# Performance work log

Hardware: AMD Instinct MI355X
Metric: run time of the kernel (lower is better)

## Reference

```python
import jax, jax.numpy as jnp
import numpy as np

D = 768      # feature_dim
HD = 768     # hidden_dim
NH = 4       # num_heads
B, T1, T2 = 4, 128, 128
LN_EPS = 1e-5

def setup_inputs() -> dict:
    key = jax.random.key(0)
    ks = jax.random.split(key, 12)
    s = 0.02
    return {
        'speech_features': jax.random.normal(ks[0], (B, T1, D), jnp.float32),
        'phoneme_features': jax.random.normal(ks[1], (B, T2, D), jnp.float32),
        # per-head attention MLP: Linear(2D->HD), ReLU, Linear(HD->1); stacked over heads
        'W1': jax.random.normal(ks[2], (NH, 2 * D, HD), jnp.float32) * s,
        'b1': jnp.zeros((NH, HD), jnp.float32),
        'w2': jax.random.normal(ks[3], (NH, HD), jnp.float32) * s,
        'b2': jnp.zeros((NH,), jnp.float32),
        # fusion: Linear(2D->2HD), ReLU, Linear(2HD->D), LayerNorm(D)
        'Wf1': jax.random.normal(ks[4], (2 * D, 2 * HD), jnp.float32) * s,
        'bf1': jnp.zeros((2 * HD,), jnp.float32),
        'Wf2': jax.random.normal(ks[5], (2 * HD, D), jnp.float32) * s,
        'bf2': jnp.zeros((D,), jnp.float32),
        'ln_g': jnp.ones((D,), jnp.float32),
        'ln_b': jnp.zeros((D,), jnp.float32),
    }

def reference(speech_features, phoneme_features, W1, b1, w2, b2, Wf1, bf1, Wf2, bf2, ln_g, ln_b):
    d = speech_features.shape[-1]
    # Decompose Linear(cat([speech_t, phoneme])) = speech@W1[:d] + phoneme@W1[d:] + b1
    Wx, Wy = W1[:, :d, :], W1[:, d:, :]
    sx = jnp.einsum('btd,ndh->nbth', speech_features, Wx)   # [NH,B,T1,HD]
    py = jnp.einsum('bsd,ndh->nbsh', phoneme_features, Wy)  # [NH,B,T2,HD]
    hidden = jax.nn.relu(sx[:, :, :, None, :] + py[:, :, None, :, :]
                         + b1[:, None, None, None, :])      # [NH,B,T1,T2,HD]
    scores = jnp.einsum('nbtsh,nh->nbts', hidden, w2) + b2[:, None, None, None]
    attn = jax.nn.softmax(scores, axis=-1).mean(axis=0)     # [B,T1,T2]
    context = jnp.einsum('bts,bsd->btd', attn, phoneme_features)  # [B,T1,D]
    fused = jnp.concatenate([speech_features, context], axis=-1)  # [B,T1,2D]
    # dropout is identity in eval mode
    h = jax.nn.relu(fused @ Wf1 + bf1)
    out = h @ Wf2 + bf2
    mu = out.mean(axis=-1, keepdims=True)
    var = ((out - mu) ** 2).mean(axis=-1, keepdims=True)
    out = (out - mu) * jax.lax.rsqrt(var + LN_EPS) * ln_g + ln_b
    return out.mean(axis=1)  # [B,D]
```

## Files before the change

kernel.cpp:

```cpp
#include <hip/hip_runtime.h>
#include <cstddef>


#define D_  768
#define HD_ 768
#define NH_ 4
#define B_  4
#define T1_ 128
#define T2_ 128
#define M_  (B_*T1_)
#define LN_EPS_ 1e-5f

typedef unsigned short u16;
typedef unsigned int u32;
typedef _Float16 f16;
typedef _Float16 f16x2 __attribute__((ext_vector_type(2)));
typedef __bf16 bf16x8 __attribute__((ext_vector_type(8)));
typedef float f32x4 __attribute__((ext_vector_type(4)));

__device__ __forceinline__ u16 f2bf(float f) {
    union { float f; unsigned int u; } v; v.f = f;
    unsigned int u = v.u + (0x7FFFu + ((v.u >> 16) & 1u));
    return (u16)(u >> 16);
}
__device__ __forceinline__ u32 pack_bf2(float lo, float hi) {
    return (u32)f2bf(lo) | ((u32)f2bf(hi) << 16);
}
__device__ __forceinline__ u16 f16bits(f16 h) {
    return __builtin_bit_cast(unsigned short, h);
}
__device__ __forceinline__ f16x2 bcast2(u32 u) {
    return __builtin_bit_cast(f16x2, u);
}
__device__ __forceinline__ u32 splat2(u16 h) { return (u32)h * 0x10001u; }

template<bool RELU, int MODE, bool AF32, bool SPLIT>
__device__ __forceinline__ void gemm_mfma_body(
    const void* __restrict__ Av1, const void* __restrict__ Av2, int lda,
    const u16* __restrict__ Bt, int ldb,
    const float* __restrict__ bias,
    void* __restrict__ C, int ldc, int K, int m0, int n0)
{
    __shared__ __align__(16) u16 As[64][40];
    __shared__ __align__(16) u16 Bs[64][40];
    __shared__ u16 Ts[MODE == 3 ? 64 : 1][MODE == 3 ? 68 : 1];

    const int tid = threadIdx.x;
    const int row = tid >> 2;
    const int kq  = (tid & 3) << 3;
    const int lane = tid & 63;
    const int w  = tid >> 6;
    const int wr = (w >> 1) << 5;
    const int wc = (w & 1) << 5;
    const int l16 = lane & 15;
    const int lk8 = (lane >> 4) << 3;
    const int r4  = (lane >> 4) << 2;

    const u16*   aptr16  = (const u16*)Av1 + (size_t)(m0 + row) * lda + kq;
    const float* aptrf1  = (const float*)Av1 + (size_t)(m0 + row) * lda + kq;
    const float* aptrf2  = SPLIT ? ((const float*)Av2 + (size_t)(m0 + row) * lda + kq) : nullptr;
    const u16*   bptr    = Bt + (size_t)(n0 + row) * ldb + kq;

    f32x4 acc00 = {0.f,0.f,0.f,0.f}, acc01 = {0.f,0.f,0.f,0.f};
    f32x4 acc10 = {0.f,0.f,0.f,0.f}, acc11 = {0.f,0.f,0.f,0.f};

    auto loadA = [&](int k0) -> uint4 {
        if (AF32) {
            const float* base = aptrf1;
            int kk = k0;
            if (SPLIT && k0 >= 768) { base = aptrf2; kk = k0 - 768; }
            float4 ax = *(const float4*)(base + kk);
            float4 ay = *(const float4*)(base + kk + 4);
            uint4 r;
            r.x = pack_bf2(ax.x, ax.y); r.y = pack_bf2(ax.z, ax.w);
            r.z = pack_bf2(ay.x, ay.y); r.w = pack_bf2(ay.z, ay.w);
            return r;
        }
        return *(const uint4*)(aptr16 + k0);
    };

    uint4 a_nxt = loadA(0);
    uint4 b_nxt = *(const uint4*)bptr;

    for (int k0 = 0; k0 < K; k0 += 32) {
        __syncthreads();
        *(uint4*)&As[row][kq] = a_nxt;
        *(uint4*)&Bs[row][kq] = b_nxt;
        if (k0 + 32 < K) {
            a_nxt = loadA(k0 + 32);
            b_nxt = *(const uint4*)(bptr + k0 + 32);
        }
        __syncthreads();
        bf16x8 af0 = *(const bf16x8*)&As[wr + l16][lk8];
        bf16x8 af1 = *(const bf16x8*)&As[wr + 16 + l16][lk8];
        bf16x8 bf0 = *(const bf16x8*)&Bs[wc + l16][lk8];
        bf16x8 bf1 = *(const bf16x8*)&Bs[wc + 16 + l16][lk8];
        acc00 = __builtin_amdgcn_mfma_f32_16x16x32_bf16(af0, bf0, acc00, 0, 0, 0);
        acc01 = __builtin_amdgcn_mfma_f32_16x16x32_bf16(af0, bf1, acc01, 0, 0, 0);
        acc10 = __builtin_amdgcn_mfma_f32_16x16x32_bf16(af1, bf0, acc10, 0, 0, 0);
        acc11 = __builtin_amdgcn_mfma_f32_16x16x32_bf16(af1, bf1, acc11, 0, 0, 0);
    }

#define EPI_FRAG(ACC, MF, NF)                                                  \
    {                                                                          \
        const int gcol = n0 + wc + (NF)*16 + l16;                              \
        const float bv = bias ? bias[gcol] : 0.f;                              \
        float v_[4];                                                           \
        _Pragma("unroll")                                                      \
        for (int r = 0; r < 4; r++) {                                          \
            float v = ACC[r] + bv;                                             \
            if (RELU) v = fmaxf(v, 0.f);                                       \
            v_[r] = v;                                                         \
        }                                                                      \
        const int lr0 = wr + (MF)*16 + r4;                                     \
        if (MODE == 3) {                                                       \
            const int lc = wc + (NF)*16 + l16;                                 \
            _Pragma("unroll")                                                  \
            for (int r = 0; r < 4; r++) Ts[lc][lr0 + r] = f16bits((f16)v_[r]); \
        } else {                                                               \
            _Pragma("unroll")                                                  \
            for (int r = 0; r < 4; r++) {                                      \
                const size_t off = (size_t)(m0 + lr0 + r) * ldc + gcol;        \
                if (MODE == 0) ((float*)C)[off] = v_[r];                       \
                else if (MODE == 1) ((u16*)C)[off] = f2bf(v_[r]);              \
                else ((u16*)C)[off] = f16bits((f16)v_[r]);                     \
            }                                                                  \
        }                                                                      \
    }
    EPI_FRAG(acc00, 0, 0) EPI_FRAG(acc01, 0, 1)
    EPI_FRAG(acc10, 1, 0) EPI_FRAG(acc11, 1, 1)
#undef EPI_FRAG

    if (MODE == 3) {
        __syncthreads();
        u16* cb = (u16*)C + (size_t)(m0 >> 7) * (768 * 128) + (m0 & 127);
#pragma unroll
        for (int u = 0; u < 4; u++) {
            const int i = tid + u * 256;
            const int hl = i >> 4;
            const int s4 = (i & 15) << 2;
            ushort4 o;
            o.x = Ts[hl][s4 + 0]; o.y = Ts[hl][s4 + 1];
            o.z = Ts[hl][s4 + 2]; o.w = Ts[hl][s4 + 3];
            *(ushort4*)(cb + (size_t)(n0 + hl) * 128 + s4) = o;
        }
    }
}

__global__ __launch_bounds__(256) void prep_kernel(
    const float* __restrict__ W1, const float* __restrict__ Wf1,
    const float* __restrict__ Wf2,
    u16* __restrict__ w1t, u16* __restrict__ wf1t, u16* __restrict__ wf2t)
{
    const int tid = threadIdx.x;
    int bid = blockIdx.x;
    const float* in; u16* outp; int tx, ty;
    if (bid < 4608) {
        const int z = bid / 1152, r = bid % 1152;
        tx = r % 24; ty = r / 24;
        in = W1 + (size_t)z * 1536 * 768; outp = w1t + (size_t)z * 768 * 1536;
    } else if (bid < 6912) {
        const int r = bid - 4608;
        tx = r % 48; ty = r / 48;
        in = Wf1; outp = wf1t;
    } else {
        const int r = bid - 6912;
        tx = r % 24; ty = r / 24;
        in = Wf2; outp = wf2t;
    }
    const int C = (bid >= 4608 && bid < 6912) ? 1536 : 768;
    const int c0 = tx * 32, r0 = ty * 32;
    __shared__ float tile[32][33];
    const int tr = tid >> 3, tc = (tid & 7) << 2;
    float4 v = *(const float4*)(in + (size_t)(r0 + tr) * C + c0 + tc);
    tile[tr][tc] = v.x; tile[tr][tc + 1] = v.y;
    tile[tr][tc + 2] = v.z; tile[tr][tc + 3] = v.w;
    __syncthreads();
    ushort4 o;
    o.x = f2bf(tile[tc + 0][tr]); o.y = f2bf(tile[tc + 1][tr]);
    o.z = f2bf(tile[tc + 2][tr]); o.w = f2bf(tile[tc + 3][tr]);
    *(ushort4*)(outp + (size_t)(c0 + tr) * 1536 + r0 + tc) = o;
}

__global__ __launch_bounds__(256) void gemm_sxpy_kernel(
    const float* __restrict__ sp, const float* __restrict__ ph,
    const u16* __restrict__ w1t, const float* __restrict__ b1,
    u16* __restrict__ sxf, u16* __restrict__ pyt)
{
    const int z = blockIdx.z;
    const int n = z & 3;
    const bool ispy = z >= 4;
    const u16* Bt = w1t + (size_t)n * 768 * 1536 + (ispy ? 768 : 0);
    if (!ispy) {
        gemm_mfma_body<false, 2, true, false>(sp, nullptr, 768, Bt, 1536, b1 + n * HD_,
                                              sxf + (size_t)n * M_ * HD_, HD_, 768,
                                              blockIdx.y * 64, blockIdx.x * 64);
    } else {
        gemm_mfma_body<false, 3, true, false>(ph, nullptr, 768, Bt, 1536, nullptr,
                                              pyt + (size_t)n * 4 * 768 * 128, 0, 768,
                                              blockIdx.y * 64, blockIdx.x * 64);
    }
}

__global__ __launch_bounds__(256) void gemm_ffn1_kernel(
    const float* __restrict__ speech, const float* __restrict__ ctx,
    const u16* __restrict__ wf1t, const float* __restrict__ bf1,
    u16* __restrict__ hbuf)
{
    gemm_mfma_body<true, 1, true, true>(speech, ctx, 768, wf1t, 1536, bf1,
                                        hbuf, 1536, 1536,
                                        blockIdx.y * 64, blockIdx.x * 64);
}

__global__ __launch_bounds__(256) void gemm_ffn2_kernel(
    const u16* __restrict__ hbuf, const u16* __restrict__ wf2t,
    const float* __restrict__ bf2, float* __restrict__ outpre)
{
    gemm_mfma_body<false, 0, false, false>(hbuf, nullptr, 1536, wf2t, 1536, bf2,
                                           outpre, 768, 1536,
                                           blockIdx.y * 64, blockIdx.x * 64);
}

__global__ __launch_bounds__(256) void scores_softmax_kernel(
    const u16* __restrict__ sxf,
    const u16* __restrict__ pyt,
    const float* __restrict__ w2,
    float* __restrict__ probs)
{
    const int bid = blockIdx.x;
    const int n = bid >> 6, b = (bid >> 4) & 3, t0 = (bid & 15) * 8;
    const int tid = threadIdx.x, lane = tid & 63, w = tid >> 6;

    __shared__ __align__(16) f16x2 sxs[8][768];
    __shared__ __align__(16) f16x2 w2s[768];

    for (int q = 0; q < 6; q++) {
        const int u = tid + q * 256;
        const int r = u / 192;
        const int h4 = (u % 192) * 4;
        ushort4 v = *(const ushort4*)(sxf + ((size_t)(n * 512 + b * 128 + t0 + r)) * 768 + h4);
        sxs[r][h4 + 0] = bcast2(splat2(v.x));
        sxs[r][h4 + 1] = bcast2(splat2(v.y));
        sxs[r][h4 + 2] = bcast2(splat2(v.z));
        sxs[r][h4 + 3] = bcast2(splat2(v.w));
    }
    for (int q = 0; q < 3; q++) {
        const int i = tid + q * 256;
        w2s[i] = bcast2(splat2(f16bits((f16)w2[n * 768 + i])));
    }
    __syncthreads();

    const f16x2* pypanel = (const f16x2*)(pyt + ((size_t)((n << 2) | b)) * 768 * 128) + lane;
    const f16x2 z2 = {(f16)0, (f16)0};

    float accA0 = 0.f, accA1 = 0.f, accB0 = 0.f, accB1 = 0.f;
    const int rA = 2 * w, rB = 2 * w + 1;

    f16x2 b0[16], b1[16];
#pragma unroll
    for (int j = 0; j < 16; j++) b0[j] = pypanel[(size_t)j * 64];
#pragma unroll
    for (int j = 0; j < 16; j++) b1[j] = pypanel[(size_t)(16 + j) * 64];

    auto compute = [&](const f16x2 (&buf)[16], int hbase) {
        f16x2 aA = z2, aB = z2;
#pragma unroll
        for (int j4 = 0; j4 < 16; j4 += 4) {
            uint4 sau = *(const uint4*)&sxs[rA][hbase + j4];
            uint4 sbu = *(const uint4*)&sxs[rB][hbase + j4];
            uint4 wvu = *(const uint4*)&w2s[hbase + j4];
            const u32 sa_[4] = {sau.x, sau.y, sau.z, sau.w};
            const u32 sb_[4] = {sbu.x, sbu.y, sbu.z, sbu.w};
            const u32 wv_[4] = {wvu.x, wvu.y, wvu.z, wvu.w};
#pragma unroll
            for (int j = 0; j < 4; j++) {
                const f16x2 pv = buf[j4 + j];
                const f16x2 wj = bcast2(wv_[j]);
                f16x2 ra = __builtin_elementwise_max(bcast2(sa_[j]) + pv, z2);
                f16x2 rb = __builtin_elementwise_max(bcast2(sb_[j]) + pv, z2);
                aA = __builtin_elementwise_fma(ra, wj, aA);
                aB = __builtin_elementwise_fma(rb, wj, aB);
            }
        }
        accA0 += (float)aA.x; accA1 += (float)aA.y;
        accB0 += (float)aB.x; accB1 += (float)aB.y;
    };

    for (int hc = 0; hc < 768; hc += 32) {
        compute(b0, hc);
        if (hc + 32 < 768) {
#pragma unroll
            for (int j = 0; j < 16; j++) b0[j] = pypanel[(size_t)(hc + 32 + j) * 64];
        }
        compute(b1, hc + 16);
        if (hc + 48 < 768) {
#pragma unroll
            for (int j = 0; j < 16; j++) b1[j] = pypanel[(size_t)(hc + 48 + j) * 64];
        }
    }

#pragma unroll
    for (int which = 0; which < 2; which++) {
        const float s0 = which ? accB0 : accA0;
        const float s1 = which ? accB1 : accA1;
        const int t = t0 + 2 * w + which;
        float mx = fmaxf(s0, s1);
#pragma unroll
        for (int off = 32; off; off >>= 1) mx = fmaxf(mx, __shfl_xor(mx, off, 64));
        const float e0 = expf(s0 - mx), e1 = expf(s1 - mx);
        float sm = e0 + e1;
#pragma unroll
        for (int off = 32; off; off >>= 1) sm += __shfl_xor(sm, off, 64);
        const float inv = 0.25f / sm;
        float2 pr; pr.x = e0 * inv; pr.y = e1 * inv;
        *(float2*)&probs[((size_t)(n * 512 + b * 128 + t)) * 128 + 2 * lane] = pr;
    }
}

__global__ __launch_bounds__(256) void context_kernel(
    const float* __restrict__ probs, const float* __restrict__ phon,
    float* __restrict__ ctx)
{
    const int m = blockIdx.x;
    const int b = m >> 7;
    const int tid = threadIdx.x;
    __shared__ float attn[T2_];
    if (tid < T2_) {
        float a = 0.f;
#pragma unroll
        for (int n = 0; n < NH_; n++)
            a += probs[(size_t)(n * M_ + m) * T2_ + tid];
        attn[tid] = a;
    }
    __syncthreads();
    const float* ph = phon + (size_t)b * T2_ * D_;
#pragma unroll
    for (int j = 0; j < 3; j++) {
        const int d = tid + 256 * j;
        float acc = 0.f;
#pragma unroll 8
        for (int s = 0; s < T2_; s++)
            acc = fmaf(attn[s], ph[(size_t)s * D_ + d], acc);
        ctx[(size_t)m * D_ + d] = acc;
    }
}

__global__ __launch_bounds__(256) void ln_fused_kernel(
    const float* __restrict__ x, const float* __restrict__ g,
    const float* __restrict__ lb, float* __restrict__ out)
{
    const int b = blockIdx.x / 3, c = blockIdx.x % 3;
    const int tid = threadIdx.x, lane = tid & 63, w = tid >> 6;
    __shared__ float rs[T1_];
    __shared__ float Sred[4];

    float prsum = 0.f;
    for (int i = 0; i < 32; i++) {
        const int row = w * 32 + i;
        const float4* x4 = (const float4*)(x + ((size_t)(b * T1_ + row)) * D_);
        float s = 0.f, ss = 0.f;
#pragma unroll
        for (int j = 0; j < 3; j++) {
            float4 v = x4[j * 64 + lane];
            s += v.x + v.y + v.z + v.w;
            ss += v.x * v.x + v.y * v.y + v.z * v.z + v.w * v.w;
        }
#pragma unroll
        for (int off = 32; off; off >>= 1) {
            s += __shfl_xor(s, off, 64);
            ss += __shfl_xor(ss, off, 64);
        }
        if (lane == 0) {
            const float mu = s * (1.f / D_);
            const float var = ss * (1.f / D_) - mu * mu;
            const float r = rsqrtf(var + LN_EPS_);
            rs[row] = r;
            prsum += mu * r;
        }
    }
    if (lane == 0) Sred[w] = prsum;
    __syncthreads();
    const float S = Sred[0] + Sred[1] + Sred[2] + Sred[3];
    const float* xb = x + (size_t)b * T1_ * D_;
    const int d = c * 256 + tid;
    float acc = 0.f;
#pragma unroll 8
    for (int t = 0; t < T1_; t++)
        acc = fmaf(xb[(size_t)t * D_ + d], rs[t], acc);
    out[b * D_ + d] = g[d] * (acc - S) * (1.f / T1_) + lb[d];
}

extern "C" void kernel_launch(void* const* d_in, const int* in_sizes, int n_in,
                              void* d_out, int out_size, void* d_ws, size_t ws_size,
                              hipStream_t stream)
{
    const float* speech = (const float*)d_in[0];
    const float* phon   = (const float*)d_in[1];
    const float* W1     = (const float*)d_in[2];
    const float* b1     = (const float*)d_in[3];
    const float* w2     = (const float*)d_in[4];
    const float* Wf1    = (const float*)d_in[6];
    const float* bf1    = (const float*)d_in[7];
    const float* Wf2    = (const float*)d_in[8];
    const float* bf2    = (const float*)d_in[9];
    const float* ln_g   = (const float*)d_in[10];
    const float* ln_b   = (const float*)d_in[11];
    float* out = (float*)d_out;

    char* w = (char*)d_ws;
    auto alloc = [&](size_t bytes) { char* p = w; w += (bytes + 1023) & ~(size_t)1023; return p; };
    u16* w1t    = (u16*)alloc((size_t)NH_ * 768 * 1536 * 2);
    u16* wf1t   = (u16*)alloc((size_t)1536 * 1536 * 2);
    u16* wf2t   = (u16*)alloc((size_t)768 * 1536 * 2);
    u16* sxf    = (u16*)alloc((size_t)NH_ * M_ * HD_ * 2);
    u16* pyt    = (u16*)alloc((size_t)NH_ * B_ * 768 * 128 * 2);
    float* probs  = (float*)alloc((size_t)NH_ * M_ * T2_ * 4);
    float* ctxb   = (float*)alloc((size_t)M_ * D_ * 4);
    u16* hbuf   = (u16*)alloc((size_t)M_ * 2 * HD_ * 2);
    float* outpre = (float*)alloc((size_t)M_ * D_ * 4);

    hipLaunchKernelGGL(prep_kernel, dim3(8064), dim3(256), 0, stream,
                       W1, Wf1, Wf2, w1t, wf1t, wf2t);
    hipLaunchKernelGGL(gemm_sxpy_kernel, dim3(HD_ / 64, M_ / 64, 8), dim3(256), 0, stream,
                       speech, phon, w1t, b1, sxf, pyt);
    hipLaunchKernelGGL(scores_softmax_kernel, dim3(256), dim3(256), 0, stream,
                       sxf, pyt, w2, probs);
    hipLaunchKernelGGL(context_kernel, dim3(M_), dim3(256), 0, stream,
                       probs, phon, ctxb);
    hipLaunchKernelGGL(gemm_ffn1_kernel, dim3(2 * HD_ / 64, M_ / 64), dim3(256), 0, stream,
                       speech, ctxb, wf1t, bf1, hbuf);
    hipLaunchKernelGGL(gemm_ffn2_kernel, dim3(D_ / 64, M_ / 64), dim3(256), 0, stream,
                       hbuf, wf2t, bf2, outpre);
    hipLaunchKernelGGL(ln_fused_kernel, dim3(12), dim3(256), 0, stream,
                       outpre, ln_g, ln_b, out);
}
```

Before: 142.6 us.

## Reassociate context@Wf1 as attn@(phoneme@Wf1y) and drop context kernel

Instead of computing context = attn @ phoneme and then feeding it through the second half of Wf1 (K=768), the code precomputes per-batch P = phoneme @ Wf1[768:] in the first GEMM launch and makes FFN1 consume the head-summed attention probabilities directly (K=128). This removes the context kernel, its fp32 buffer, and shrinks the FFN1 reduction from 1536 to 896, at the cost of an extra 4x128x1536 GEMM and rounding the attention weights and P to bf16. The sx, py and new P GEMMs are merged into one flat-grid launch.

Result: faster. 129.5 us (-9.2%).

```diff
diff --git a/kernel.cpp b/kernel.cpp
--- a/kernel.cpp
+++ b/kernel.cpp
@@ -34,16 +34,16 @@
 }
 __device__ __forceinline__ u32 splat2(u16 h) { return (u32)h * 0x10001u; }
 
-template<bool RELU, int MODE, bool AF32, bool SPLIT>
+template<bool RELU, int MODE, bool AF32>
 __device__ __forceinline__ void gemm_mfma_body(
-    const void* __restrict__ Av1, const void* __restrict__ Av2, int lda,
+    const void* __restrict__ Av, int lda,
     const u16* __restrict__ Bt, int ldb,
     const float* __restrict__ bias,
     void* __restrict__ C, int ldc, int K, int m0, int n0)
 {
     __shared__ __align__(16) u16 As[64][40];
     __shared__ __align__(16) u16 Bs[64][40];
-    __shared__ u16 Ts[MODE == 3 ? 64 : 1][MODE == 3 ? 68 : 1];
+    __shared__ u16 Ts[MODE >= 3 ? 64 : 1][MODE >= 3 ? 68 : 1];
 
     const int tid = threadIdx.x;
     const int row = tid >> 2;
@@ -56,21 +56,17 @@
     const int lk8 = (lane >> 4) << 3;
     const int r4  = (lane >> 4) << 2;
 
-    const u16*   aptr16  = (const u16*)Av1 + (size_t)(m0 + row) * lda + kq;
-    const float* aptrf1  = (const float*)Av1 + (size_t)(m0 + row) * lda + kq;
-    const float* aptrf2  = SPLIT ? ((const float*)Av2 + (size_t)(m0 + row) * lda + kq) : nullptr;
-    const u16*   bptr    = Bt + (size_t)(n0 + row) * ldb + kq;
+    const u16*   aptr16 = (const u16*)Av + (size_t)(m0 + row) * lda + kq;
+    const float* aptrf  = (const float*)Av + (size_t)(m0 + row) * lda + kq;
+    const u16*   bptr   = Bt + (size_t)(n0 + row) * ldb + kq;
 
     f32x4 acc00 = {0.f,0.f,0.f,0.f}, acc01 = {0.f,0.f,0.f,0.f};
     f32x4 acc10 = {0.f,0.f,0.f,0.f}, acc11 = {0.f,0.f,0.f,0.f};
 
     auto loadA = [&](int k0) -> uint4 {
         if (AF32) {
-            const float* base = aptrf1;
-            int kk = k0;
-            if (SPLIT && k0 >= 768) { base = aptrf2; kk = k0 - 768; }
-            float4 ax = *(const float4*)(base + kk);
-            float4 ay = *(const float4*)(base + kk + 4);
+            float4 ax = *(const float4*)(aptrf + k0);
+            float4 ay = *(const float4*)(aptrf + k0 + 4);
             uint4 r;
             r.x = pack_bf2(ax.x, ax.y); r.y = pack_bf2(ax.z, ax.w);
             r.z = pack_bf2(ay.x, ay.y); r.w = pack_bf2(ay.z, ay.w);
@@ -113,10 +109,12 @@
             v_[r] = v;                                                         \
         }                                                                      \
         const int lr0 = wr + (MF)*16 + r4;                                     \
-        if (MODE == 3) {                                                       \
+        if (MODE >= 3) {                                                       \
             const int lc = wc + (NF)*16 + l16;                                 \
             _Pragma("unroll")                                                  \
-            for (int r = 0; r < 4; r++) Ts[lc][lr0 + r] = f16bits((f16)v_[r]); \
+            for (int r = 0; r < 4; r++)                                        \
+                Ts[lc][lr0 + r] = (MODE == 3) ? f16bits((f16)v_[r])            \
+                                              : f2bf(v_[r]);                   \
         } else {                                                               \
             _Pragma("unroll")                                                  \
             for (int r = 0; r < 4; r++) {                                      \
@@ -131,9 +129,9 @@
     EPI_FRAG(acc10, 1, 0) EPI_FRAG(acc11, 1, 1)
 #undef EPI_FRAG
 
-    if (MODE == 3) {
+    if (MODE >= 3) {
         __syncthreads();
-        u16* cb = (u16*)C + (size_t)(m0 >> 7) * (768 * 128) + (m0 & 127);
+        u16* cb = (u16*)C + (size_t)(m0 >> 7) * ((size_t)ldc * 128) + (m0 & 127);
 #pragma unroll
         for (int u = 0; u < 4; u++) {
             const int i = tid + u * 256;
@@ -182,43 +180,31 @@
     *(ushort4*)(outp + (size_t)(c0 + tr) * 1536 + r0 + tc) = o;
 }
 
-__global__ __launch_bounds__(256) void gemm_sxpy_kernel(
+__global__ __launch_bounds__(256) void sxpypw_kernel(
     const float* __restrict__ sp, const float* __restrict__ ph,
-    const u16* __restrict__ w1t, const float* __restrict__ b1,
-    u16* __restrict__ sxf, u16* __restrict__ pyt)
-{
-    const int z = blockIdx.z;
-    const int n = z & 3;
-    const bool ispy = z >= 4;
-    const u16* Bt = w1t + (size_t)n * 768 * 1536 + (ispy ? 768 : 0);
-    if (!ispy) {
-        gemm_mfma_body<false, 2, true, false>(sp, nullptr, 768, Bt, 1536, b1 + n * HD_,
-                                              sxf + (size_t)n * M_ * HD_, HD_, 768,
-                                              blockIdx.y * 64, blockIdx.x * 64);
+    const u16* __restrict__ w1t, const u16* __restrict__ wf1t,
+    const float* __restrict__ b1,
+    u16* __restrict__ sxf, u16* __restrict__ pyt, u16* __restrict__ pwt)
+{
+    int job = blockIdx.x;
+    if (job < 384) {
+        const int n = job / 96, r = job % 96, my = r / 12, nx = r % 12;
+        gemm_mfma_body<false, 2, true>(sp, 768,
+            w1t + (size_t)n * 768 * 1536, 1536, b1 + n * HD_,
+            sxf + (size_t)n * M_ * HD_, HD_, 768, my * 64, nx * 64);
+    } else if (job < 768) {
+        const int j = job - 384;
+        const int n = j / 96, r = j % 96, my = r / 12, nx = r % 12;
+        gemm_mfma_body<false, 3, true>(ph, 768,
+            w1t + (size_t)n * 768 * 1536 + 768, 1536, nullptr,
+            pyt + (size_t)n * 4 * 768 * 128, 768, 768, my * 64, nx * 64);
     } else {
-        gemm_mfma_body<false, 3, true, false>(ph, nullptr, 768, Bt, 1536, nullptr,
-                                              pyt + (size_t)n * 4 * 768 * 128, 0, 768,
-                                              blockIdx.y * 64, blockIdx.x * 64);
-    }
-}
-
-__global__ __launch_bounds__(256) void gemm_ffn1_kernel(
-    const float* __restrict__ speech, const float* __restrict__ ctx,
-    const u16* __restrict__ wf1t, const float* __restrict__ bf1,
-    u16* __restrict__ hbuf)
-{
-    gemm_mfma_body<true, 1, true, true>(speech, ctx, 768, wf1t, 1536, bf1,
-                                        hbuf, 1536, 1536,
-                                        blockIdx.y * 64, blockIdx.x * 64);
-}
-
-__global__ __launch_bounds__(256) void gemm_ffn2_kernel(
-    const u16* __restrict__ hbuf, const u16* __restrict__ wf2t,
-    const float* __restrict__ bf2, float* __restrict__ outpre)
-{
-    gemm_mfma_body<false, 0, false, false>(hbuf, nullptr, 1536, wf2t, 1536, bf2,
-                                           outpre, 768, 1536,
-                                           blockIdx.y * 64, blockIdx.x * 64);
+        const int j = job - 768;
+        const int b = j / 48, r = j % 48, my = r / 24, nx = r % 24;
+        gemm_mfma_body<false, 4, true>(ph + (size_t)b * 128 * 768, 768,
+            wf1t + 768, 1536, nullptr,
+            pwt + (size_t)b * 1536 * 128, 1536, 768, my * 64, nx * 64);
+    }
 }
 
 __global__ __launch_bounds__(256) void scores_softmax_kernel(
@@ -317,32 +303,108 @@
     }
 }
 
-__global__ __launch_bounds__(256) void context_kernel(
-    const float* __restrict__ probs, const float* __restrict__ phon,
-    float* __restrict__ ctx)
-{
-    const int m = blockIdx.x;
-    const int b = m >> 7;
+__global__ __launch_bounds__(256) void gemm_ffn1_kernel(
+    const float* __restrict__ speech, const float* __restrict__ probs,
+    const u16* __restrict__ wf1t, const u16* __restrict__ pwt,
+    const float* __restrict__ bf1, u16* __restrict__ hbuf)
+{
+    __shared__ __align__(16) u16 As[64][40];
+    __shared__ __align__(16) u16 Bs[64][40];
+
     const int tid = threadIdx.x;
-    __shared__ float attn[T2_];
-    if (tid < T2_) {
-        float a = 0.f;
-#pragma unroll
-        for (int n = 0; n < NH_; n++)
-            a += probs[(size_t)(n * M_ + m) * T2_ + tid];
-        attn[tid] = a;
-    }
-    __syncthreads();
-    const float* ph = phon + (size_t)b * T2_ * D_;
-#pragma unroll
-    for (int j = 0; j < 3; j++) {
-        const int d = tid + 256 * j;
-        float acc = 0.f;
-#pragma unroll 8
-        for (int s = 0; s < T2_; s++)
-            acc = fmaf(attn[s], ph[(size_t)s * D_ + d], acc);
-        ctx[(size_t)m * D_ + d] = acc;
-    }
+    const int row = tid >> 2;
+    const int kq  = (tid & 3) << 3;
+    const int lane = tid & 63;
+    const int w  = tid >> 6;
+    const int wr = (w >> 1) << 5;
+    const int wc = (w & 1) << 5;
+    const int l16 = lane & 15;
+    const int lk8 = (lane >> 4) << 3;
+    const int r4  = (lane >> 4) << 2;
+
+    const int m0 = blockIdx.y * 64, n0 = blockIdx.x * 64;
+    const int b = m0 >> 7;
+
+    const float* arow = speech + (size_t)(m0 + row) * 768 + kq;
+    const float* prow = probs + (size_t)(m0 + row) * 128 + kq;
+    const u16* brow_w = wf1t + (size_t)(n0 + row) * 1536 + kq;
+    const u16* brow_p = pwt + (size_t)b * 1536 * 128 + (size_t)(n0 + row) * 128 + kq;
+
+    f32x4 acc00 = {0.f,0.f,0.f,0.f}, acc01 = {0.f,0.f,0.f,0.f};
+    f32x4 acc10 = {0.f,0.f,0.f,0.f}, acc11 = {0.f,0.f,0.f,0.f};
+
+    auto loadA = [&](int k0) -> uint4 {
+        uint4 r;
+        if (k0 < 768) {
+            float4 ax = *(const float4*)(arow + k0);
+            float4 ay = *(const float4*)(arow + k0 + 4);
+            r.x = pack_bf2(ax.x, ax.y); r.y = pack_bf2(ax.z, ax.w);
+            r.z = pack_bf2(ay.x, ay.y); r.w = pack_bf2(ay.z, ay.w);
+        } else {
+            const int ko = k0 - 768;
+            float4 ax = make_float4(0.f, 0.f, 0.f, 0.f), ay = ax;
+#pragma unroll
+            for (int n = 0; n < 4; n++) {
+                float4 u0 = *(const float4*)(prow + (size_t)n * 512 * 128 + ko);
+                float4 u1 = *(const float4*)(prow + (size_t)n * 512 * 128 + ko + 4);
+                ax.x += u0.x; ax.y += u0.y; ax.z += u0.z; ax.w += u0.w;
+                ay.x += u1.x; ay.y += u1.y; ay.z += u1.z; ay.w += u1.w;
+            }
+            r.x = pack_bf2(ax.x, ax.y); r.y = pack_bf2(ax.z, ax.w);
+            r.z = pack_bf2(ay.x, ay.y); r.w = pack_bf2(ay.z, ay.w);
+        }
+        return r;
+    };
+    auto loadB = [&](int k0) -> uint4 {
+        if (k0 < 768) return *(const uint4*)(brow_w + k0);
+        return *(const uint4*)(brow_p + (k0 - 768));
+    };
+
+    uint4 a_nxt = loadA(0);
+    uint4 b_nxt = loadB(0);
+
+    for (int k0 = 0; k0 < 896; k0 += 32) {
+        __syncthreads();
+        *(uint4*)&As[row][kq] = a_nxt;
+        *(uint4*)&Bs[row][kq] = b_nxt;
+        if (k0 + 32 < 896) {
+            a_nxt = loadA(k0 + 32);
+            b_nxt = loadB(k0 + 32);
+        }
+        __syncthreads();
+        bf16x8 af0 = *(const bf16x8*)&As[wr + l16][lk8];
+        bf16x8 af1 = *(const bf16x8*)&As[wr + 16 + l16][lk8];
+        bf16x8 bf0 = *(const bf16x8*)&Bs[wc + l16][lk8];
+        bf16x8 bf1 = *(const bf16x8*)&Bs[wc + 16 + l16][lk8];
+        acc00 = __builtin_amdgcn_mfma_f32_16x16x32_bf16(af0, bf0, acc00, 0, 0, 0);
+        acc01 = __builtin_amdgcn_mfma_f32_16x16x32_bf16(af0, bf1, acc01, 0, 0, 0);
+        acc10 = __builtin_amdgcn_mfma_f32_16x16x32_bf16(af1, bf0, acc10, 0, 0, 0);
+        acc11 = __builtin_amdgcn_mfma_f32_16x16x32_bf16(af1, bf1, acc11, 0, 0, 0);
+    }
+
+#define EPI_FFN1(ACC, MF, NF)                                                  \
+    {                                                                          \
+        const int gcol = n0 + wc + (NF)*16 + l16;                              \
+        const float bv = bf1[gcol];                                            \
+        const int lr0 = wr + (MF)*16 + r4;                                     \
+        _Pragma("unroll")                                                      \
+        for (int r = 0; r < 4; r++) {                                          \
+            float v = fmaxf(ACC[r] + bv, 0.f);                                 \
+            hbuf[(size_t)(m0 + lr0 + r) * 1536 + gcol] = f2bf(v);              \
+        }                                                                      \
+    }
+    EPI_FFN1(acc00, 0, 0) EPI_FFN1(acc01, 0, 1)
+    EPI_FFN1(acc10, 1, 0) EPI_FFN1(acc11, 1, 1)
+#undef EPI_FFN1
+}
+
+__global__ __launch_bounds__(256) void gemm_ffn2_kernel(
+    const u16* __restrict__ hbuf, const u16* __restrict__ wf2t,
+    const float* __restrict__ bf2, float* __restrict__ outpre)
+{
+    gemm_mfma_body<false, 0, false>(hbuf, 1536, wf2t, 1536, bf2,
+                                    outpre, 768, 1536,
+                                    blockIdx.y * 64, blockIdx.x * 64);
 }
 
 __global__ __launch_bounds__(256) void ln_fused_kernel(
@@ -414,22 +476,20 @@
     u16* wf2t   = (u16*)alloc((size_t)768 * 1536 * 2);
     u16* sxf    = (u16*)alloc((size_t)NH_ * M_ * HD_ * 2);
     u16* pyt    = (u16*)alloc((size_t)NH_ * B_ * 768 * 128 * 2);
+    u16* pwt    = (u16*)alloc((size_t)B_ * 1536 * 128 * 2);
     float* probs  = (float*)alloc((size_t)NH_ * M_ * T2_ * 4);
-    float* ctxb   = (float*)alloc((size_t)M_ * D_ * 4);
     u16* hbuf   = (u16*)alloc((size_t)M_ * 2 * HD_ * 2);
     float* outpre = (float*)alloc((size_t)M_ * D_ * 4);
 
     hipLaunchKernelGGL(prep_kernel, dim3(8064), dim3(256), 0, stream,
                        W1, Wf1, Wf2, w1t, wf1t, wf2t);
-    hipLaunchKernelGGL(gemm_sxpy_kernel, dim3(HD_ / 64, M_ / 64, 8), dim3(256), 0, stream,
-                       speech, phon, w1t, b1, sxf, pyt);
+    hipLaunchKernelGGL(sxpypw_kernel, dim3(960), dim3(256), 0, stream,
+                       speech, phon, w1t, wf1t, b1, sxf, pyt, pwt);
     hipLaunchKernelGGL(scores_softmax_kernel, dim3(256), dim3(256), 0, stream,
                        sxf, pyt, w2, probs);
-    hipLaunchKernelGGL(context_kernel, dim3(M_), dim3(256), 0, stream,
-                       probs, phon, ctxb);
-    hipLaunchKernelGGL(gemm_ffn1_kernel, dim3(2 * HD_ / 64, M_ / 64), dim3(256), 0, stream,
-                       speech, ctxb, wf1t, bf1, hbuf);
-    hipLaunchKernelGGL(gemm_ffn2_kernel, dim3(D_ / 64, M_ / 64), dim3(256), 0, stream,
+    hipLaunchKernelGGL(gemm_ffn1_kernel, dim3(24, 8), dim3(256), 0, stream,
+                       speech, probs, wf1t, pwt, bf1, hbuf);
+    hipLaunchKernelGGL(gemm_ffn2_kernel, dim3(12, 8), dim3(256), 0, stream,
                        hbuf, wf2t, bf2, outpre);
     hipLaunchKernelGGL(ln_fused_kernel, dim3(12), dim3(256), 0, stream,
                        outpre, ln_g, ln_b, out);
```
